# Optimization experiments

Hardware: AMD Instinct MI355X
Metric: run time of the kernel (lower is better)

## Reference

```python
import jax, jax.numpy as jnp
import numpy as np


def setup_inputs() -> dict:
    key = jax.random.key(0)
    k1, k2, k3, k4 = jax.random.split(key, 4)
    B, D, N = 4, 128, 512
    scale = 1.0 / np.sqrt(2 * D)  # conv fan_in = 2D
    x = jax.random.normal(k1, (B, D, N), dtype=jnp.float32)
    W1 = jax.random.normal(k2, (D, D), dtype=jnp.float32) * scale  # acts on (x_j - x_i)
    W2 = jax.random.normal(k3, (D, D), dtype=jnp.float32) * scale  # acts on x_i
    b = jax.random.normal(k4, (D,), dtype=jnp.float32) * scale
    return {"x": x, "W1": W1, "W2": W2, "b": b}


def reference(x, W1, W2, b):
    # Original: feature[b, :, i, j] = concat(x_j - x_i, x_i); 1x1 conv (weight [D, 2D]);
    # ReLU; max over j. The 1x1 conv is linear, so with W = [W1 | W2]:
    #   pre[b, d, i, j] = (W1 x_j)[d] - (W1 x_i)[d] + (W2 x_i)[d] + b[d]
    A = jnp.einsum('od,bdn->bon', W1, x)               # [B, D, N]  W1 @ x_n
    C = jnp.einsum('od,bdn->bon', W2, x) + b[None, :, None]  # [B, D, N]
    # pre: [B, D, N(i), N(j)]
    pre = A[:, :, None, :] + (C - A)[:, :, :, None]
    out = jnp.max(jax.nn.relu(pre), axis=-1)           # max over neighbors j -> [B, D, N]
    return out
```

## Files before the change

### kernel.cpp

```cpp
#include <hip/hip_runtime.h>
#include <hip/hip_bf16.h>

#define PB 4
#define PD 128
#define PN 512

__device__ __forceinline__ float f4get(const float4& v, int k) {
  const float* p = (const float*)&v;
  return p[k];
}

__global__ __launch_bounds__(256) void gcn_one(
    const float* __restrict__ x, const float* __restrict__ W1,
    const float* __restrict__ W2, const float* __restrict__ bias,
    float* __restrict__ out) {
  const int bid = blockIdx.x;
  const int b = bid >> 6;
  const int r0 = (bid & 63) << 1;
  const int tid = threadIdx.x;
  const int lane = tid & 63;
  const int w = tid >> 6;

  __shared__ float4 ws[2][2][32];
  __shared__ float redmax[2][4];

  if (tid < 128) {
    const int mat = tid >> 6;
    const int r = (tid >> 5) & 1;
    const int c = tid & 31;
    const float* Wm = mat ? W2 : W1;
    ws[mat][r][c] = *(const float4*)(Wm + (size_t)(r0 + r) * PD + (c << 2));
  }
  __syncthreads();

  const int n0 = (w << 7) + (lane << 1);
  const float* xp = x + (size_t)b * PD * PN + n0;

  float2 a0 = {0.f, 0.f}, a1 = {0.f, 0.f};
  float2 c0 = {0.f, 0.f}, c1 = {0.f, 0.f};

#pragma unroll 4
  for (int dc = 0; dc < 32; ++dc) {
    const float4 w10 = ws[0][0][dc];
    const float4 w11 = ws[0][1][dc];
    const float4 w20 = ws[1][0][dc];
    const float4 w21 = ws[1][1][dc];
    float2 xv[4];
#pragma unroll
    for (int k = 0; k < 4; ++k)
      xv[k] = *(const float2*)(xp + (size_t)(dc * 4 + k) * PN);
#pragma unroll
    for (int k = 0; k < 4; ++k) {
      const float u10 = f4get(w10, k), u11 = f4get(w11, k);
      const float u20 = f4get(w20, k), u21 = f4get(w21, k);
      a0.x = fmaf(u10, xv[k].x, a0.x); a0.y = fmaf(u10, xv[k].y, a0.y);
      a1.x = fmaf(u11, xv[k].x, a1.x); a1.y = fmaf(u11, xv[k].y, a1.y);
      c0.x = fmaf(u20, xv[k].x, c0.x); c0.y = fmaf(u20, xv[k].y, c0.y);
      c1.x = fmaf(u21, xv[k].x, c1.x); c1.y = fmaf(u21, xv[k].y, c1.y);
    }
  }

  float m0 = fmaxf(a0.x, a0.y);
  float m1 = fmaxf(a1.x, a1.y);
#pragma unroll
  for (int off = 32; off > 0; off >>= 1) {
    m0 = fmaxf(m0, __shfl_xor(m0, off));
    m1 = fmaxf(m1, __shfl_xor(m1, off));
  }
  if (lane == 0) {
    redmax[0][w] = m0;
    redmax[1][w] = m1;
  }
  __syncthreads();
  const float M0 = fmaxf(fmaxf(redmax[0][0], redmax[0][1]),
                         fmaxf(redmax[0][2], redmax[0][3]));
  const float M1 = fmaxf(fmaxf(redmax[1][0], redmax[1][1]),
                         fmaxf(redmax[1][2], redmax[1][3]));
  const float b0 = bias[r0], b1 = bias[r0 + 1];

  float2 o0, o1;
  o0.x = fmaxf(M0 + c0.x + b0 - a0.x, 0.f);
  o0.y = fmaxf(M0 + c0.y + b0 - a0.y, 0.f);
  o1.x = fmaxf(M1 + c1.x + b1 - a1.x, 0.f);
  o1.y = fmaxf(M1 + c1.y + b1 - a1.y, 0.f);

  float* op = out + (size_t)(b * PD + r0) * PN + n0;
  *(float2*)op = o0;
  *(float2*)(op + PN) = o1;
}

extern "C" void kernel_launch(void* const* d_in, const int* in_sizes, int n_in,
                              void* d_out, int out_size, void* d_ws, size_t ws_size,
                              hipStream_t stream) {
  const float* x = (const float*)d_in[0];
  const float* W1 = (const float*)d_in[1];
  const float* W2 = (const float*)d_in[2];
  const float* bias = (const float*)d_in[3];
  float* out = (float*)d_out;

  gcn_one<<<dim3(PB * PD / 2), dim3(256), 0, stream>>>(x, W1, W2, bias, out);
}
```

Baseline: 11.91 us.

## Split reduction dimension across four thread groups with float4 loads

```diff
diff --git a/kernel.cpp b/kernel.cpp
--- a/kernel.cpp
+++ b/kernel.cpp
@@ -10,7 +10,7 @@
   return p[k];
 }
 
-__global__ __launch_bounds__(256) void gcn_one(
+__global__ __launch_bounds__(512) void gcn_one(
     const float* __restrict__ x, const float* __restrict__ W1,
     const float* __restrict__ W2, const float* __restrict__ bias,
     float* __restrict__ out) {
@@ -18,11 +18,12 @@
   const int b = bid >> 6;
   const int r0 = (bid & 63) << 1;
   const int tid = threadIdx.x;
-  const int lane = tid & 63;
-  const int w = tid >> 6;
+  const int g = tid >> 7;
+  const int t = tid & 127;
 
   __shared__ float4 ws[2][2][32];
-  __shared__ float redmax[2][4];
+  __shared__ float4 red[3][4][128];
+  __shared__ float rmax[2][2];
 
   if (tid < 128) {
     const int mat = tid >> 6;
@@ -33,60 +34,86 @@
   }
   __syncthreads();
 
-  const int n0 = (w << 7) + (lane << 1);
-  const float* xp = x + (size_t)b * PD * PN + n0;
+  const float* xp = x + (size_t)b * PD * PN + (size_t)(g << 5) * PN + (t << 2);
 
-  float2 a0 = {0.f, 0.f}, a1 = {0.f, 0.f};
-  float2 c0 = {0.f, 0.f}, c1 = {0.f, 0.f};
+  float4 a0 = {0.f, 0.f, 0.f, 0.f}, a1 = a0, c0 = a0, c1 = a0;
 
-#pragma unroll 4
-  for (int dc = 0; dc < 32; ++dc) {
-    const float4 w10 = ws[0][0][dc];
-    const float4 w11 = ws[0][1][dc];
-    const float4 w20 = ws[1][0][dc];
-    const float4 w21 = ws[1][1][dc];
-    float2 xv[4];
+#pragma unroll
+  for (int dc = 0; dc < 8; ++dc) {
+    const float4 w10 = ws[0][0][(g << 3) + dc];
+    const float4 w11 = ws[0][1][(g << 3) + dc];
+    const float4 w20 = ws[1][0][(g << 3) + dc];
+    const float4 w21 = ws[1][1][(g << 3) + dc];
+    float4 xv[4];
 #pragma unroll
     for (int k = 0; k < 4; ++k)
-      xv[k] = *(const float2*)(xp + (size_t)(dc * 4 + k) * PN);
+      xv[k] = *(const float4*)(xp + (size_t)((dc << 2) + k) * PN);
 #pragma unroll
     for (int k = 0; k < 4; ++k) {
       const float u10 = f4get(w10, k), u11 = f4get(w11, k);
       const float u20 = f4get(w20, k), u21 = f4get(w21, k);
       a0.x = fmaf(u10, xv[k].x, a0.x); a0.y = fmaf(u10, xv[k].y, a0.y);
+      a0.z = fmaf(u10, xv[k].z, a0.z); a0.w = fmaf(u10, xv[k].w, a0.w);
       a1.x = fmaf(u11, xv[k].x, a1.x); a1.y = fmaf(u11, xv[k].y, a1.y);
+      a1.z = fmaf(u11, xv[k].z, a1.z); a1.w = fmaf(u11, xv[k].w, a1.w);
       c0.x = fmaf(u20, xv[k].x, c0.x); c0.y = fmaf(u20, xv[k].y, c0.y);
+      c0.z = fmaf(u20, xv[k].z, c0.z); c0.w = fmaf(u20, xv[k].w, c0.w);
       c1.x = fmaf(u21, xv[k].x, c1.x); c1.y = fmaf(u21, xv[k].y, c1.y);
+      c1.z = fmaf(u21, xv[k].z, c1.z); c1.w = fmaf(u21, xv[k].w, c1.w);
     }
   }
 
-  float m0 = fmaxf(a0.x, a0.y);
-  float m1 = fmaxf(a1.x, a1.y);
-#pragma unroll
-  for (int off = 32; off > 0; off >>= 1) {
-    m0 = fmaxf(m0, __shfl_xor(m0, off));
-    m1 = fmaxf(m1, __shfl_xor(m1, off));
-  }
-  if (lane == 0) {
-    redmax[0][w] = m0;
-    redmax[1][w] = m1;
+  if (g > 0) {
+    red[g - 1][0][t] = a0;
+    red[g - 1][1][t] = a1;
+    red[g - 1][2][t] = c0;
+    red[g - 1][3][t] = c1;
   }
   __syncthreads();
-  const float M0 = fmaxf(fmaxf(redmax[0][0], redmax[0][1]),
-                         fmaxf(redmax[0][2], redmax[0][3]));
-  const float M1 = fmaxf(fmaxf(redmax[1][0], redmax[1][1]),
-                         fmaxf(redmax[1][2], redmax[1][3]));
-  const float b0 = bias[r0], b1 = bias[r0 + 1];
 
-  float2 o0, o1;
-  o0.x = fmaxf(M0 + c0.x + b0 - a0.x, 0.f);
-  o0.y = fmaxf(M0 + c0.y + b0 - a0.y, 0.f);
-  o1.x = fmaxf(M1 + c1.x + b1 - a1.x, 0.f);
-  o1.y = fmaxf(M1 + c1.y + b1 - a1.y, 0.f);
+  if (g == 0) {
+#pragma unroll
+    for (int gg = 0; gg < 3; ++gg) {
+      const float4 ra0 = red[gg][0][t], ra1 = red[gg][1][t];
+      const float4 rc0 = red[gg][2][t], rc1 = red[gg][3][t];
+      a0.x += ra0.x; a0.y += ra0.y; a0.z += ra0.z; a0.w += ra0.w;
+      a1.x += ra1.x; a1.y += ra1.y; a1.z += ra1.z; a1.w += ra1.w;
+      c0.x += rc0.x; c0.y += rc0.y; c0.z += rc0.z; c0.w += rc0.w;
+      c1.x += rc1.x; c1.y += rc1.y; c1.z += rc1.z; c1.w += rc1.w;
+    }
+    float m0 = fmaxf(fmaxf(a0.x, a0.y), fmaxf(a0.z, a0.w));
+    float m1 = fmaxf(fmaxf(a1.x, a1.y), fmaxf(a1.z, a1.w));
+#pragma unroll
+    for (int off = 32; off > 0; off >>= 1) {
+      m0 = fmaxf(m0, __shfl_xor(m0, off));
+      m1 = fmaxf(m1, __shfl_xor(m1, off));
+    }
+    if ((t & 63) == 0) {
+      rmax[0][t >> 6] = m0;
+      rmax[1][t >> 6] = m1;
+    }
+  }
+  __syncthreads();
 
-  float* op = out + (size_t)(b * PD + r0) * PN + n0;
-  *(float2*)op = o0;
-  *(float2*)(op + PN) = o1;
+  if (g == 0) {
+    const float M0 = fmaxf(rmax[0][0], rmax[0][1]);
+    const float M1 = fmaxf(rmax[1][0], rmax[1][1]);
+    const float b0 = bias[r0], b1 = bias[r0 + 1];
+
+    float4 o0, o1;
+    o0.x = fmaxf(M0 + c0.x + b0 - a0.x, 0.f);
+    o0.y = fmaxf(M0 + c0.y + b0 - a0.y, 0.f);
+    o0.z = fmaxf(M0 + c0.z + b0 - a0.z, 0.f);
+    o0.w = fmaxf(M0 + c0.w + b0 - a0.w, 0.f);
+    o1.x = fmaxf(M1 + c1.x + b1 - a1.x, 0.f);
+    o1.y = fmaxf(M1 + c1.y + b1 - a1.y, 0.f);
+    o1.z = fmaxf(M1 + c1.z + b1 - a1.z, 0.f);
+    o1.w = fmaxf(M1 + c1.w + b1 - a1.w, 0.f);
+
+    float* op = out + (size_t)(b * PD + r0) * PN + (t << 2);
+    *(float4*)op = o0;
+    *(float4*)(op + PN) = o1;
+  }
 }
 
 extern "C" void kernel_launch(void* const* d_in, const int* in_sizes, int n_in,
@@ -98,5 +125,5 @@
   const float* bias = (const float*)d_in[3];
   float* out = (float*)d_out;
 
-  gcn_one<<<dim3(PB * PD / 2), dim3(256), 0, stream>>>(x, W1, W2, bias, out);
+  gcn_one<<<dim3(PB * PD / 2), dim3(512), 0, stream>>>(x, W1, W2, bias, out);
 }
```

Result: slower. 12.55 us (+5.4%).

## Split reduction dimension across two thread halves with 512-thread blocks

Applied to the files above, without the earlier changes.

```diff
diff --git a/kernel.cpp b/kernel.cpp
--- a/kernel.cpp
+++ b/kernel.cpp
@@ -10,7 +10,7 @@
   return p[k];
 }
 
-__global__ __launch_bounds__(256) void gcn_one(
+__global__ __launch_bounds__(512) void gcn_one(
     const float* __restrict__ x, const float* __restrict__ W1,
     const float* __restrict__ W2, const float* __restrict__ bias,
     float* __restrict__ out) {
@@ -18,75 +18,76 @@
   const int b = bid >> 6;
   const int r0 = (bid & 63) << 1;
   const int tid = threadIdx.x;
-  const int lane = tid & 63;
-  const int w = tid >> 6;
+  const int t = tid & 127;
+  const int r = (tid >> 7) & 1;
+  const int dh = tid >> 8;
 
   __shared__ float4 ws[2][2][32];
-  __shared__ float redmax[2][4];
+  __shared__ float4 red[2][128][2];
+  __shared__ float rmax[2][2];
 
   if (tid < 128) {
     const int mat = tid >> 6;
-    const int r = (tid >> 5) & 1;
+    const int rr = (tid >> 5) & 1;
     const int c = tid & 31;
     const float* Wm = mat ? W2 : W1;
-    ws[mat][r][c] = *(const float4*)(Wm + (size_t)(r0 + r) * PD + (c << 2));
+    ws[mat][rr][c] = *(const float4*)(Wm + (size_t)(r0 + rr) * PD + (c << 2));
   }
   __syncthreads();
 
-  const int n0 = (w << 7) + (lane << 1);
-  const float* xp = x + (size_t)b * PD * PN + n0;
+  const float* xp = x + (size_t)b * PD * PN + (size_t)(dh << 6) * PN + (t << 2);
 
-  float2 a0 = {0.f, 0.f}, a1 = {0.f, 0.f};
-  float2 c0 = {0.f, 0.f}, c1 = {0.f, 0.f};
+  float4 a = {0.f, 0.f, 0.f, 0.f};
+  float4 c = {0.f, 0.f, 0.f, 0.f};
 
 #pragma unroll 4
-  for (int dc = 0; dc < 32; ++dc) {
-    const float4 w10 = ws[0][0][dc];
-    const float4 w11 = ws[0][1][dc];
-    const float4 w20 = ws[1][0][dc];
-    const float4 w21 = ws[1][1][dc];
-    float2 xv[4];
+  for (int dc = 0; dc < 16; ++dc) {
+    const int chunk = (dh << 4) + dc;
+    const float4 w1v = ws[0][r][chunk];
+    const float4 w2v = ws[1][r][chunk];
+    float4 xv[4];
 #pragma unroll
     for (int k = 0; k < 4; ++k)
-      xv[k] = *(const float2*)(xp + (size_t)(dc * 4 + k) * PN);
+      xv[k] = *(const float4*)(xp + (size_t)((dc << 2) + k) * PN);
 #pragma unroll
     for (int k = 0; k < 4; ++k) {
-      const float u10 = f4get(w10, k), u11 = f4get(w11, k);
-      const float u20 = f4get(w20, k), u21 = f4get(w21, k);
-      a0.x = fmaf(u10, xv[k].x, a0.x); a0.y = fmaf(u10, xv[k].y, a0.y);
-      a1.x = fmaf(u11, xv[k].x, a1.x); a1.y = fmaf(u11, xv[k].y, a1.y);
-      c0.x = fmaf(u20, xv[k].x, c0.x); c0.y = fmaf(u20, xv[k].y, c0.y);
-      c1.x = fmaf(u21, xv[k].x, c1.x); c1.y = fmaf(u21, xv[k].y, c1.y);
+      const float u1 = f4get(w1v, k), u2 = f4get(w2v, k);
+      a.x = fmaf(u1, xv[k].x, a.x); a.y = fmaf(u1, xv[k].y, a.y);
+      a.z = fmaf(u1, xv[k].z, a.z); a.w = fmaf(u1, xv[k].w, a.w);
+      c.x = fmaf(u2, xv[k].x, c.x); c.y = fmaf(u2, xv[k].y, c.y);
+      c.z = fmaf(u2, xv[k].z, c.z); c.w = fmaf(u2, xv[k].w, c.w);
     }
   }
 
-  float m0 = fmaxf(a0.x, a0.y);
-  float m1 = fmaxf(a1.x, a1.y);
-#pragma unroll
-  for (int off = 32; off > 0; off >>= 1) {
-    m0 = fmaxf(m0, __shfl_xor(m0, off));
-    m1 = fmaxf(m1, __shfl_xor(m1, off));
-  }
-  if (lane == 0) {
-    redmax[0][w] = m0;
-    redmax[1][w] = m1;
+  if (dh == 1) {
+    red[r][t][0] = a;
+    red[r][t][1] = c;
   }
   __syncthreads();
-  const float M0 = fmaxf(fmaxf(redmax[0][0], redmax[0][1]),
-                         fmaxf(redmax[0][2], redmax[0][3]));
-  const float M1 = fmaxf(fmaxf(redmax[1][0], redmax[1][1]),
-                         fmaxf(redmax[1][2], redmax[1][3]));
-  const float b0 = bias[r0], b1 = bias[r0 + 1];
 
-  float2 o0, o1;
-  o0.x = fmaxf(M0 + c0.x + b0 - a0.x, 0.f);
-  o0.y = fmaxf(M0 + c0.y + b0 - a0.y, 0.f);
-  o1.x = fmaxf(M1 + c1.x + b1 - a1.x, 0.f);
-  o1.y = fmaxf(M1 + c1.y + b1 - a1.y, 0.f);
+  if (dh == 0) {
+    const float4 ra = red[r][t][0], rc = red[r][t][1];
+    a.x += ra.x; a.y += ra.y; a.z += ra.z; a.w += ra.w;
+    c.x += rc.x; c.y += rc.y; c.z += rc.z; c.w += rc.w;
 
-  float* op = out + (size_t)(b * PD + r0) * PN + n0;
-  *(float2*)op = o0;
-  *(float2*)(op + PN) = o1;
+    float m = fmaxf(fmaxf(a.x, a.y), fmaxf(a.z, a.w));
+#pragma unroll
+    for (int off = 32; off > 0; off >>= 1)
+      m = fmaxf(m, __shfl_xor(m, off));
+    if ((t & 63) == 0) rmax[r][t >> 6] = m;
+  }
+  __syncthreads();
+
+  if (dh == 0) {
+    const float M = fmaxf(rmax[r][0], rmax[r][1]);
+    const float bv = bias[r0 + r];
+    float4 o;
+    o.x = fmaxf(M + c.x + bv - a.x, 0.f);
+    o.y = fmaxf(M + c.y + bv - a.y, 0.f);
+    o.z = fmaxf(M + c.z + bv - a.z, 0.f);
+    o.w = fmaxf(M + c.w + bv - a.w, 0.f);
+    *(float4*)(out + (size_t)(b * PD + r0 + r) * PN + (t << 2)) = o;
+  }
 }
 
 extern "C" void kernel_launch(void* const* d_in, const int* in_sizes, int n_in,
@@ -98,5 +99,5 @@
   const float* bias = (const float*)d_in[3];
   float* out = (float*)d_out;
 
-  gcn_one<<<dim3(PB * PD / 2), dim3(256), 0, stream>>>(x, W1, W2, bias, out);
+  gcn_one<<<dim3(PB * PD / 2), dim3(512), 0, stream>>>(x, W1, W2, bias, out);
 }
```

Measured after the change: 10.97 us (median of 2 runs). 7.9% less time.
